# Optimization experiments

Hardware: AMD Instinct MI355X
Metric: run time of the kernel (lower is better)

Reference implementation:

```python
import jax, jax.numpy as jnp
import numpy as np

B, N, D, L = 4, 512, 128, 2


def setup_inputs() -> dict:
    key = jax.random.key(0)
    ks = jax.random.split(key, 6)
    node_feats = jax.random.normal(ks[0], (B, N, D), dtype=jnp.float32)
    adj_mask = jax.random.uniform(ks[1], (B, N, N), dtype=jnp.float32)
    # torch Linear weights: [out_features, in_features]
    w1 = jax.random.normal(ks[2], (L, D, 2 * D), dtype=jnp.float32) * 0.05
    b1 = jax.random.normal(ks[3], (L, D), dtype=jnp.float32) * 0.05
    w2 = jax.random.normal(ks[4], (L, D, D), dtype=jnp.float32) * 0.05
    b2 = jax.random.normal(ks[5], (L, D), dtype=jnp.float32) * 0.05
    return {"node_feats": node_feats, "adj_mask": adj_mask,
            "w1": w1, "b1": b1, "w2": w2, "b2": b2}


def reference(node_feats, adj_mask, w1, b1, w2, b2):
    h = node_feats
    d = h.shape[-1]
    n_layers = w1.shape[0]
    for l in range(n_layers):
        # cat([hi, hj]) @ W1^T == hi @ Wi^T + hj @ Wj^T  (avoid 2D concat)
        wi = w1[l][:, :d]   # [D, D]
        wj = w1[l][:, d:]   # [D, D]
        ai = jnp.einsum('bnd,od->bno', h, wi)  # contribution of node i
        aj = jnp.einsum('bnd,od->bno', h, wj)  # contribution of node j
        # [B, N(i), N(j), D]
        m = jax.nn.relu(ai[:, :, None, :] + aj[:, None, :, :] + b1[l])
        m = jnp.einsum('bijd,od->bijo', m, w2[l]) + b2[l]
        m = m * adj_mask[..., None]
        msg = m.sum(axis=2)  # sum over j
        h = h + msg
    return h
```

## Files before the change

### kernel.cpp

```cpp
#include <hip/hip_runtime.h>


constexpr int Bc = 4, Nc = 512, Dc = 128, Lc = 2;
constexpr int BN = Bc * Nc;
constexpr int TIB = 4;
constexpr int TN = 4;

__global__ void transpose_w_kernel(const float* __restrict__ w1,
                                   const float* __restrict__ w2,
                                   float* __restrict__ wiT,
                                   float* __restrict__ wjT,
                                   float* __restrict__ w2T) {
    int idx = blockIdx.x * blockDim.x + threadIdx.x;
    if (idx >= Lc * Dc * Dc) return;
    int l = idx / (Dc * Dc);
    int rem = idx - l * Dc * Dc;
    int d = rem / Dc;
    int o = rem - d * Dc;
    wiT[idx] = w1[(l * Dc + o) * (2 * Dc) + d];
    wjT[idx] = w1[(l * Dc + o) * (2 * Dc) + Dc + d];
    w2T[idx] = w2[(l * Dc + o) * Dc + d];
}

__global__ __launch_bounds__(128) void gnn_lin1(const float* __restrict__ h,
                                                const float* __restrict__ wiT,
                                                const float* __restrict__ wjT,
                                                const float* __restrict__ b1,
                                                float* __restrict__ ai,
                                                float* __restrict__ aj) {
    __shared__ float hs[TN][Dc];
    const int o = threadIdx.x;
    const int r0 = blockIdx.x * TN;
#pragma unroll
    for (int t = 0; t < TN; ++t) hs[t][o] = h[(r0 + t) * Dc + o];
    __syncthreads();
    float acci[TN], accj[TN];
    const float bo = b1[o];
#pragma unroll
    for (int t = 0; t < TN; ++t) { acci[t] = bo; accj[t] = 0.f; }
    for (int d = 0; d < Dc; d += 4) {
        float wi[4], wj[4];
#pragma unroll
        for (int k = 0; k < 4; ++k) {
            wi[k] = wiT[(d + k) * Dc + o];
            wj[k] = wjT[(d + k) * Dc + o];
        }
#pragma unroll
        for (int t = 0; t < TN; ++t) {
            const float4 hv = *reinterpret_cast<const float4*>(&hs[t][d]);
            acci[t] = fmaf(hv.x, wi[0], acci[t]);
            acci[t] = fmaf(hv.y, wi[1], acci[t]);
            acci[t] = fmaf(hv.z, wi[2], acci[t]);
            acci[t] = fmaf(hv.w, wi[3], acci[t]);
            accj[t] = fmaf(hv.x, wj[0], accj[t]);
            accj[t] = fmaf(hv.y, wj[1], accj[t]);
            accj[t] = fmaf(hv.z, wj[2], accj[t]);
            accj[t] = fmaf(hv.w, wj[3], accj[t]);
        }
    }
#pragma unroll
    for (int t = 0; t < TN; ++t) {
        ai[(r0 + t) * Dc + o] = acci[t];
        aj[(r0 + t) * Dc + o] = accj[t];
    }
}

template <bool HAS_NEXT>
__global__ __launch_bounds__(512) void gnn_msgfull(
    const float* __restrict__ ai, const float* __restrict__ aj,
    const float* __restrict__ adj, const float* __restrict__ hin,
    const float* __restrict__ w2T, const float* __restrict__ b2,
    const float* __restrict__ wiT, const float* __restrict__ wjT,
    const float* __restrict__ b1, float* __restrict__ hout,
    float* __restrict__ ai_out, float* __restrict__ aj_out) {
    __shared__ __align__(16) float adjs[TIB][Nc];
    __shared__ __align__(16) float scratch[4096];
    __shared__ float s_lds[TIB][Dc];
    __shared__ float hnew_lds[TIB][Dc];
    __shared__ float redw[8];

    const int tid = threadIdx.x;
    const int w = tid >> 6;
    const int lane = tid & 63;
    const int r0 = blockIdx.x * TIB;
    const int b = r0 >> 9;
    const int i0 = r0 & (Nc - 1);
    const float* __restrict__ ajb = aj + (size_t)b * Nc * Dc;
    const float* __restrict__ adjb = adj + (size_t)b * Nc * Nc;

    {
        const int rr = tid >> 7;
        const int c4 = (tid & 127) * 4;
        const float4 av =
            *reinterpret_cast<const float4*>(&adjb[(size_t)(i0 + rr) * Nc + c4]);
        *reinterpret_cast<float4*>(&adjs[rr][c4]) = av;
        float p = av.x + av.y + av.z + av.w;
#pragma unroll
        for (int m = 32; m >= 1; m >>= 1) p += __shfl_xor(p, m);
        if (lane == 0) redw[w] = p;
    }

    const int jlane = lane >> 5;
    const int dq = (lane & 31) * 4;
    float4 x[TIB], acc[TIB];
#pragma unroll
    for (int r = 0; r < TIB; ++r) {
        x[r] = *reinterpret_cast<const float4*>(&ai[(size_t)(r0 + r) * Dc + dq]);
        acc[r] = make_float4(0.f, 0.f, 0.f, 0.f);
    }
    __syncthreads();

    const int jw = w * 64;
    const float* __restrict__ pbase = ajb + (size_t)(jw + jlane) * Dc + dq;
#pragma unroll 4
    for (int it = 0; it < 32; ++it) {
        const float4 v = *reinterpret_cast<const float4*>(pbase + (size_t)it * 256);
        const int j = jw + 2 * it + jlane;
        const float a0 = adjs[0][j];
        const float a1 = adjs[1][j];
        const float a2 = adjs[2][j];
        const float a3 = adjs[3][j];
#define ROWF(r, a)                                                       \
        acc[r].x = fmaf(a, fmaxf(x[r].x + v.x, 0.f), acc[r].x);          \
        acc[r].y = fmaf(a, fmaxf(x[r].y + v.y, 0.f), acc[r].y);          \
        acc[r].z = fmaf(a, fmaxf(x[r].z + v.z, 0.f), acc[r].z);          \
        acc[r].w = fmaf(a, fmaxf(x[r].w + v.w, 0.f), acc[r].w);
        ROWF(0, a0) ROWF(1, a1) ROWF(2, a2) ROWF(3, a3)
#undef ROWF
    }

#pragma unroll
    for (int r = 0; r < TIB; ++r) {
        acc[r].x += __shfl_xor(acc[r].x, 32);
        acc[r].y += __shfl_xor(acc[r].y, 32);
        acc[r].z += __shfl_xor(acc[r].z, 32);
        acc[r].w += __shfl_xor(acc[r].w, 32);
    }
    if (lane < 32) {
#pragma unroll
        for (int r = 0; r < TIB; ++r)
            *reinterpret_cast<float4*>(&scratch[w * 512 + r * 128 + dq]) = acc[r];
    }
    __syncthreads();

    {
        const int rr = tid >> 7;
        const int dd = tid & 127;
        float s = 0.f;
#pragma unroll
        for (int ww = 0; ww < 8; ++ww) s += scratch[ww * 512 + rr * 128 + dd];
        s_lds[rr][dd] = s;
    }
    __syncthreads();

    {
        const int o = tid & 127;
        const int g = tid >> 7;
        float part[TIB] = {0.f, 0.f, 0.f, 0.f};
        for (int dd = g * 32; dd < g * 32 + 32; dd += 4) {
            float wv[4];
#pragma unroll
            for (int k = 0; k < 4; ++k) wv[k] = w2T[(size_t)(dd + k) * Dc + o];
#pragma unroll
            for (int r = 0; r < TIB; ++r) {
                const float4 sv = *reinterpret_cast<const float4*>(&s_lds[r][dd]);
                part[r] = fmaf(sv.x, wv[0], part[r]);
                part[r] = fmaf(sv.y, wv[1], part[r]);
                part[r] = fmaf(sv.z, wv[2], part[r]);
                part[r] = fmaf(sv.w, wv[3], part[r]);
            }
        }
#pragma unroll
        for (int r = 0; r < TIB; ++r) scratch[g * 512 + r * 128 + o] = part[r];
    }
    __syncthreads();

    {
        const int rr = tid >> 7;
        const int o = tid & 127;
        float a2c = scratch[rr * 128 + o] + scratch[512 + rr * 128 + o] +
                    scratch[1024 + rr * 128 + o] + scratch[1536 + rr * 128 + o];
        const float arow_r = redw[2 * rr] + redw[2 * rr + 1];
        const float hn =
            hin[(size_t)(r0 + rr) * Dc + o] + a2c + arow_r * b2[o];
        hout[(size_t)(r0 + rr) * Dc + o] = hn;
        if constexpr (HAS_NEXT) hnew_lds[rr][o] = hn;
    }

    if constexpr (HAS_NEXT) {
        __syncthreads();
        {
            const int o = tid & 127;
            const int g = tid >> 7;
            float pi[TIB] = {0.f, 0.f, 0.f, 0.f};
            float pj[TIB] = {0.f, 0.f, 0.f, 0.f};
            for (int dd = g * 32; dd < g * 32 + 32; dd += 4) {
                float wiv[4], wjv[4];
#pragma unroll
                for (int k = 0; k < 4; ++k) {
                    wiv[k] = wiT[(size_t)(dd + k) * Dc + o];
                    wjv[k] = wjT[(size_t)(dd + k) * Dc + o];
                }
#pragma unroll
                for (int r = 0; r < TIB; ++r) {
                    const float4 hv =
                        *reinterpret_cast<const float4*>(&hnew_lds[r][dd]);
                    pi[r] = fmaf(hv.x, wiv[0], pi[r]);
                    pi[r] = fmaf(hv.y, wiv[1], pi[r]);
                    pi[r] = fmaf(hv.z, wiv[2], pi[r]);
                    pi[r] = fmaf(hv.w, wiv[3], pi[r]);
                    pj[r] = fmaf(hv.x, wjv[0], pj[r]);
                    pj[r] = fmaf(hv.y, wjv[1], pj[r]);
                    pj[r] = fmaf(hv.z, wjv[2], pj[r]);
                    pj[r] = fmaf(hv.w, wjv[3], pj[r]);
                }
            }
#pragma unroll
            for (int r = 0; r < TIB; ++r) {
                scratch[g * 512 + r * 128 + o] = pi[r];
                scratch[2048 + g * 512 + r * 128 + o] = pj[r];
            }
        }
        __syncthreads();
        {
            const int rr = tid >> 7;
            const int o = tid & 127;
            float acci = b1[o];
            float accj = 0.f;
#pragma unroll
            for (int g = 0; g < 4; ++g) {
                acci += scratch[g * 512 + rr * 128 + o];
                accj += scratch[2048 + g * 512 + rr * 128 + o];
            }
            ai_out[(size_t)(r0 + rr) * Dc + o] = acci;
            aj_out[(size_t)(r0 + rr) * Dc + o] = accj;
        }
    }
}

extern "C" void kernel_launch(void* const* d_in, const int* in_sizes, int n_in,
                              void* d_out, int out_size, void* d_ws, size_t ws_size,
                              hipStream_t stream) {
    const float* node = (const float*)d_in[0];
    const float* adj  = (const float*)d_in[1];
    const float* w1   = (const float*)d_in[2];
    const float* b1   = (const float*)d_in[3];
    const float* w2   = (const float*)d_in[4];
    const float* b2   = (const float*)d_in[5];
    float* out = (float*)d_out;

    float* ws = (float*)d_ws;
    float* wiT = ws; ws += Lc * Dc * Dc;
    float* wjT = ws; ws += Lc * Dc * Dc;
    float* w2T = ws; ws += Lc * Dc * Dc;
    float* ai  = ws; ws += BN * Dc;
    float* aj  = ws; ws += BN * Dc;
    float* ai2 = ws; ws += BN * Dc;
    float* aj2 = ws; ws += BN * Dc;
    float* h1  = ws; ws += BN * Dc;

    transpose_w_kernel<<<(Lc * Dc * Dc + 255) / 256, 256, 0, stream>>>(
        w1, w2, wiT, wjT, w2T);

    gnn_lin1<<<BN / TN, 128, 0, stream>>>(node, wiT, wjT, b1, ai, aj);
    gnn_msgfull<true><<<BN / TIB, 512, 0, stream>>>(
        ai, aj, adj, node, w2T, b2, wiT + Dc * Dc, wjT + Dc * Dc, b1 + Dc,
        h1, ai2, aj2);
    gnn_msgfull<false><<<BN / TIB, 512, 0, stream>>>(
        ai2, aj2, adj, h1, w2T + Dc * Dc, b2 + Dc, nullptr, nullptr, nullptr,
        out, nullptr, nullptr);
}
```

Measured before the change: 50.71 us.

## Drop weight transpose kernel and store adjacency tile transposed in LDS

Removes the separate weight-transpose launch and reads the original row-major W1/W2 directly with per-thread float4 loads along the input dimension. The adjacency tile is now kept in LDS as [j][row], so the hot message loop fetches all four row weights with one float4 LDS read instead of four scalar reads. Row sums of the adjacency are reduced per row through a small LDS table. The cost is uncoalesced global weight loads (each thread reads a different 512B/1KB row), which must rely on cache.

Result: slower. 56.69 us (+11.8%).

```diff
diff --git a/kernel.cpp b/kernel.cpp
--- a/kernel.cpp
+++ b/kernel.cpp
@@ -6,25 +6,8 @@
 constexpr int TIB = 4;
 constexpr int TN = 4;
 
-__global__ void transpose_w_kernel(const float* __restrict__ w1,
-                                   const float* __restrict__ w2,
-                                   float* __restrict__ wiT,
-                                   float* __restrict__ wjT,
-                                   float* __restrict__ w2T) {
-    int idx = blockIdx.x * blockDim.x + threadIdx.x;
-    if (idx >= Lc * Dc * Dc) return;
-    int l = idx / (Dc * Dc);
-    int rem = idx - l * Dc * Dc;
-    int d = rem / Dc;
-    int o = rem - d * Dc;
-    wiT[idx] = w1[(l * Dc + o) * (2 * Dc) + d];
-    wjT[idx] = w1[(l * Dc + o) * (2 * Dc) + Dc + d];
-    w2T[idx] = w2[(l * Dc + o) * Dc + d];
-}
-
 __global__ __launch_bounds__(128) void gnn_lin1(const float* __restrict__ h,
-                                                const float* __restrict__ wiT,
-                                                const float* __restrict__ wjT,
+                                                const float* __restrict__ w1,
                                                 const float* __restrict__ b1,
                                                 float* __restrict__ ai,
                                                 float* __restrict__ aj) {
@@ -32,36 +15,33 @@
     const int o = threadIdx.x;
     const int r0 = blockIdx.x * TN;
 #pragma unroll
-    for (int t = 0; t < TN; ++t) hs[t][o] = h[(r0 + t) * Dc + o];
+    for (int t = 0; t < TN; ++t) hs[t][o] = h[(size_t)(r0 + t) * Dc + o];
     __syncthreads();
     float acci[TN], accj[TN];
     const float bo = b1[o];
 #pragma unroll
     for (int t = 0; t < TN; ++t) { acci[t] = bo; accj[t] = 0.f; }
+    const float* __restrict__ w1row = w1 + (size_t)o * (2 * Dc);
     for (int d = 0; d < Dc; d += 4) {
-        float wi[4], wj[4];
-#pragma unroll
-        for (int k = 0; k < 4; ++k) {
-            wi[k] = wiT[(d + k) * Dc + o];
-            wj[k] = wjT[(d + k) * Dc + o];
-        }
+        const float4 wi = *reinterpret_cast<const float4*>(&w1row[d]);
+        const float4 wj = *reinterpret_cast<const float4*>(&w1row[Dc + d]);
 #pragma unroll
         for (int t = 0; t < TN; ++t) {
             const float4 hv = *reinterpret_cast<const float4*>(&hs[t][d]);
-            acci[t] = fmaf(hv.x, wi[0], acci[t]);
-            acci[t] = fmaf(hv.y, wi[1], acci[t]);
-            acci[t] = fmaf(hv.z, wi[2], acci[t]);
-            acci[t] = fmaf(hv.w, wi[3], acci[t]);
-            accj[t] = fmaf(hv.x, wj[0], accj[t]);
-            accj[t] = fmaf(hv.y, wj[1], accj[t]);
-            accj[t] = fmaf(hv.z, wj[2], accj[t]);
-            accj[t] = fmaf(hv.w, wj[3], accj[t]);
+            acci[t] = fmaf(hv.x, wi.x, acci[t]);
+            acci[t] = fmaf(hv.y, wi.y, acci[t]);
+            acci[t] = fmaf(hv.z, wi.z, acci[t]);
+            acci[t] = fmaf(hv.w, wi.w, acci[t]);
+            accj[t] = fmaf(hv.x, wj.x, accj[t]);
+            accj[t] = fmaf(hv.y, wj.y, accj[t]);
+            accj[t] = fmaf(hv.z, wj.z, accj[t]);
+            accj[t] = fmaf(hv.w, wj.w, accj[t]);
         }
     }
 #pragma unroll
     for (int t = 0; t < TN; ++t) {
-        ai[(r0 + t) * Dc + o] = acci[t];
-        aj[(r0 + t) * Dc + o] = accj[t];
+        ai[(size_t)(r0 + t) * Dc + o] = acci[t];
+        aj[(size_t)(r0 + t) * Dc + o] = accj[t];
     }
 }
 
@@ -69,15 +49,16 @@
 __global__ __launch_bounds__(512) void gnn_msgfull(
     const float* __restrict__ ai, const float* __restrict__ aj,
     const float* __restrict__ adj, const float* __restrict__ hin,
-    const float* __restrict__ w2T, const float* __restrict__ b2,
-    const float* __restrict__ wiT, const float* __restrict__ wjT,
-    const float* __restrict__ b1, float* __restrict__ hout,
-    float* __restrict__ ai_out, float* __restrict__ aj_out) {
-    __shared__ __align__(16) float adjs[TIB][Nc];
+    const float* __restrict__ w2, const float* __restrict__ b2,
+    const float* __restrict__ w1n, const float* __restrict__ b1n,
+    float* __restrict__ hout, float* __restrict__ ai_out,
+    float* __restrict__ aj_out) {
+    __shared__ __align__(16) float adjsT[Nc][TIB];
     __shared__ __align__(16) float scratch[4096];
     __shared__ float s_lds[TIB][Dc];
     __shared__ float hnew_lds[TIB][Dc];
-    __shared__ float redw[8];
+    __shared__ float redw[8][TIB];
+    __shared__ float arow_l[TIB];
 
     const int tid = threadIdx.x;
     const int w = tid >> 6;
@@ -89,15 +70,18 @@
     const float* __restrict__ adjb = adj + (size_t)b * Nc * Nc;
 
     {
-        const int rr = tid >> 7;
-        const int c4 = (tid & 127) * 4;
-        const float4 av =
-            *reinterpret_cast<const float4*>(&adjb[(size_t)(i0 + rr) * Nc + c4]);
-        *reinterpret_cast<float4*>(&adjs[rr][c4]) = av;
-        float p = av.x + av.y + av.z + av.w;
-#pragma unroll
-        for (int m = 32; m >= 1; m >>= 1) p += __shfl_xor(p, m);
-        if (lane == 0) redw[w] = p;
+        float av[TIB];
+#pragma unroll
+        for (int r = 0; r < TIB; ++r) av[r] = adjb[(size_t)(i0 + r) * Nc + tid];
+        *reinterpret_cast<float4*>(&adjsT[tid][0]) =
+            make_float4(av[0], av[1], av[2], av[3]);
+#pragma unroll
+        for (int r = 0; r < TIB; ++r) {
+            float p = av[r];
+#pragma unroll
+            for (int m = 32; m >= 1; m >>= 1) p += __shfl_xor(p, m);
+            if (lane == 0) redw[w][r] = p;
+        }
     }
 
     const int jlane = lane >> 5;
@@ -114,18 +98,16 @@
     const float* __restrict__ pbase = ajb + (size_t)(jw + jlane) * Dc + dq;
 #pragma unroll 4
     for (int it = 0; it < 32; ++it) {
-        const float4 v = *reinterpret_cast<const float4*>(pbase + (size_t)it * 256);
-        const int j = jw + 2 * it + jlane;
-        const float a0 = adjs[0][j];
-        const float a1 = adjs[1][j];
-        const float a2 = adjs[2][j];
-        const float a3 = adjs[3][j];
+        const float4 v =
+            *reinterpret_cast<const float4*>(pbase + (size_t)it * 2 * Dc);
+        const float4 a4 =
+            *reinterpret_cast<const float4*>(&adjsT[jw + 2 * it + jlane][0]);
 #define ROWF(r, a)                                                       \
         acc[r].x = fmaf(a, fmaxf(x[r].x + v.x, 0.f), acc[r].x);          \
         acc[r].y = fmaf(a, fmaxf(x[r].y + v.y, 0.f), acc[r].y);          \
         acc[r].z = fmaf(a, fmaxf(x[r].z + v.z, 0.f), acc[r].z);          \
         acc[r].w = fmaf(a, fmaxf(x[r].w + v.w, 0.f), acc[r].w);
-        ROWF(0, a0) ROWF(1, a1) ROWF(2, a2) ROWF(3, a3)
+        ROWF(0, a4.x) ROWF(1, a4.y) ROWF(2, a4.z) ROWF(3, a4.w)
 #undef ROWF
     }
 
@@ -151,23 +133,28 @@
         for (int ww = 0; ww < 8; ++ww) s += scratch[ww * 512 + rr * 128 + dd];
         s_lds[rr][dd] = s;
     }
+    if (tid < TIB) {
+        float p = 0.f;
+#pragma unroll
+        for (int ww = 0; ww < 8; ++ww) p += redw[ww][tid];
+        arow_l[tid] = p;
+    }
     __syncthreads();
 
     {
         const int o = tid & 127;
         const int g = tid >> 7;
+        const float* __restrict__ w2row = w2 + (size_t)o * Dc;
         float part[TIB] = {0.f, 0.f, 0.f, 0.f};
         for (int dd = g * 32; dd < g * 32 + 32; dd += 4) {
-            float wv[4];
-#pragma unroll
-            for (int k = 0; k < 4; ++k) wv[k] = w2T[(size_t)(dd + k) * Dc + o];
+            const float4 wv = *reinterpret_cast<const float4*>(&w2row[dd]);
 #pragma unroll
             for (int r = 0; r < TIB; ++r) {
                 const float4 sv = *reinterpret_cast<const float4*>(&s_lds[r][dd]);
-                part[r] = fmaf(sv.x, wv[0], part[r]);
-                part[r] = fmaf(sv.y, wv[1], part[r]);
-                part[r] = fmaf(sv.z, wv[2], part[r]);
-                part[r] = fmaf(sv.w, wv[3], part[r]);
+                part[r] = fmaf(sv.x, wv.x, part[r]);
+                part[r] = fmaf(sv.y, wv.y, part[r]);
+                part[r] = fmaf(sv.z, wv.z, part[r]);
+                part[r] = fmaf(sv.w, wv.w, part[r]);
             }
         }
 #pragma unroll
@@ -180,9 +167,8 @@
         const int o = tid & 127;
         float a2c = scratch[rr * 128 + o] + scratch[512 + rr * 128 + o] +
                     scratch[1024 + rr * 128 + o] + scratch[1536 + rr * 128 + o];
-        const float arow_r = redw[2 * rr] + redw[2 * rr + 1];
         const float hn =
-            hin[(size_t)(r0 + rr) * Dc + o] + a2c + arow_r * b2[o];
+            hin[(size_t)(r0 + rr) * Dc + o] + a2c + arow_l[rr] * b2[o];
         hout[(size_t)(r0 + rr) * Dc + o] = hn;
         if constexpr (HAS_NEXT) hnew_lds[rr][o] = hn;
     }
@@ -192,27 +178,25 @@
         {
             const int o = tid & 127;
             const int g = tid >> 7;
+            const float* __restrict__ w1row = w1n + (size_t)o * (2 * Dc);
             float pi[TIB] = {0.f, 0.f, 0.f, 0.f};
             float pj[TIB] = {0.f, 0.f, 0.f, 0.f};
             for (int dd = g * 32; dd < g * 32 + 32; dd += 4) {
-                float wiv[4], wjv[4];
-#pragma unroll
-                for (int k = 0; k < 4; ++k) {
-                    wiv[k] = wiT[(size_t)(dd + k) * Dc + o];
-                    wjv[k] = wjT[(size_t)(dd + k) * Dc + o];
-                }
+                const float4 wiv = *reinterpret_cast<const float4*>(&w1row[dd]);
+                const float4 wjv =
+                    *reinterpret_cast<const float4*>(&w1row[Dc + dd]);
 #pragma unroll
                 for (int r = 0; r < TIB; ++r) {
                     const float4 hv =
                         *reinterpret_cast<const float4*>(&hnew_lds[r][dd]);
-                    pi[r] = fmaf(hv.x, wiv[0], pi[r]);
-                    pi[r] = fmaf(hv.y, wiv[1], pi[r]);
-                    pi[r] = fmaf(hv.z, wiv[2], pi[r]);
-                    pi[r] = fmaf(hv.w, wiv[3], pi[r]);
-                    pj[r] = fmaf(hv.x, wjv[0], pj[r]);
-                    pj[r] = fmaf(hv.y, wjv[1], pj[r]);
-                    pj[r] = fmaf(hv.z, wjv[2], pj[r]);
-                    pj[r] = fmaf(hv.w, wjv[3], pj[r]);
+                    pi[r] = fmaf(hv.x, wiv.x, pi[r]);
+                    pi[r] = fmaf(hv.y, wiv.y, pi[r]);
+                    pi[r] = fmaf(hv.z, wiv.z, pi[r]);
+                    pi[r] = fmaf(hv.w, wiv.w, pi[r]);
+                    pj[r] = fmaf(hv.x, wjv.x, pj[r]);
+                    pj[r] = fmaf(hv.y, wjv.y, pj[r]);
+                    pj[r] = fmaf(hv.z, wjv.z, pj[r]);
+                    pj[r] = fmaf(hv.w, wjv.w, pj[r]);
                 }
             }
 #pragma unroll
@@ -225,7 +209,7 @@
         {
             const int rr = tid >> 7;
             const int o = tid & 127;
-            float acci = b1[o];
+            float acci = b1n[o];
             float accj = 0.f;
 #pragma unroll
             for (int g = 0; g < 4; ++g) {
@@ -250,23 +234,16 @@
     float* out = (float*)d_out;
 
     float* ws = (float*)d_ws;
-    float* wiT = ws; ws += Lc * Dc * Dc;
-    float* wjT = ws; ws += Lc * Dc * Dc;
-    float* w2T = ws; ws += Lc * Dc * Dc;
     float* ai  = ws; ws += BN * Dc;
     float* aj  = ws; ws += BN * Dc;
     float* ai2 = ws; ws += BN * Dc;
     float* aj2 = ws; ws += BN * Dc;
     float* h1  = ws; ws += BN * Dc;
 
-    transpose_w_kernel<<<(Lc * Dc * Dc + 255) / 256, 256, 0, stream>>>(
-        w1, w2, wiT, wjT, w2T);
-
-    gnn_lin1<<<BN / TN, 128, 0, stream>>>(node, wiT, wjT, b1, ai, aj);
+    gnn_lin1<<<BN / TN, 128, 0, stream>>>(node, w1, b1, ai, aj);
     gnn_msgfull<true><<<BN / TIB, 512, 0, stream>>>(
-        ai, aj, adj, node, w2T, b2, wiT + Dc * Dc, wjT + Dc * Dc, b1 + Dc,
-        h1, ai2, aj2);
+        ai, aj, adj, node, w2, b2, w1 + Dc * 2 * Dc, b1 + Dc, h1, ai2, aj2);
     gnn_msgfull<false><<<BN / TIB, 512, 0, stream>>>(
-        ai2, aj2, adj, h1, w2T + Dc * Dc, b2 + Dc, nullptr, nullptr, nullptr,
-        out, nullptr, nullptr);
+        ai2, aj2, adj, h1, w2 + Dc * Dc, b2 + Dc, nullptr, nullptr, out,
+        nullptr, nullptr);
 }
```
